# Optimization experiments

Measured on AMD Instinct MI355X. Metric: run time of the kernel, lower is better.

The kernel has to match this reference:

```python
import jax, jax.numpy as jnp
import numpy as np

B, C_IN, C_OUT, H, W = 16, 64, 64, 256, 256
M1, M2 = 32, 32  # retained Fourier modes (low-frequency corner block)


def setup_inputs() -> dict:
    key = jax.random.key(0)
    kx, kw, kb = jax.random.split(key, 3)
    x = jax.random.normal(kx, (B, C_IN, H, W), dtype=jnp.float32)
    # xavier_uniform over (in, out, m1, m2): fan_in = C_IN*M1*M2, fan_out = C_OUT*M1*M2
    bound = float(np.sqrt(6.0 / ((C_IN + C_OUT) * M1 * M2)))
    weights = jax.random.uniform(kw, (C_IN, C_OUT, M1, M2), jnp.float32, -bound, bound)
    bias = jax.random.normal(kb, (C_OUT,), dtype=jnp.float32) * 0.01
    return {"x": x, "weights": weights, "bias": bias}


def reference(x, weights, bias):
    # x: [B, Cin, H, W] real -> rFFT2 -> [B, Cin, H, W//2+1] complex
    x_ft = jnp.fft.rfft2(x, axes=(-2, -1))
    m1 = min(M1, x_ft.shape[-2])
    m2 = min(M2, x_ft.shape[-1])
    # Single fused complex-times-real channel mixing over the truncated mode block
    mixed = jnp.einsum("bixy,ioxy->boxy",
                       x_ft[:, :, :m1, :m2],
                       weights[:, :, :m1, :m2].astype(x_ft.dtype))
    out_ft = jnp.zeros((x.shape[0], weights.shape[1], x_ft.shape[-2], x_ft.shape[-1]),
                       dtype=x_ft.dtype)
    out_ft = out_ft.at[:, :, :m1, :m2].set(mixed)
    x_out = jnp.fft.irfft2(out_ft, s=(x.shape[-2], x.shape[-1]), axes=(-2, -1))
    return x_out + bias[None, :, None, None]
```

## Files before the change

kernel.cpp:

```cpp
#include <hip/hip_runtime.h>


#define H_ 256
#define W_ 256

typedef short short8 __attribute__((ext_vector_type(8)));
typedef float floatx4 __attribute__((ext_vector_type(4)));

static __device__ __forceinline__ unsigned short f2b(float f) {
    union { float f; unsigned int u; } v; v.f = f;
    unsigned int r = v.u + 0x7FFFu + ((v.u >> 16) & 1u);
    return (unsigned short)(r >> 16);
}

static __device__ __forceinline__ unsigned int cvt_pk_bf16(float a, float b) {
    unsigned int r;
    asm("v_cvt_pk_bf16_f32 %0, %1, %2" : "=v"(r) : "v"(a), "v"(b));
    return r;
}

__global__ void build_tables(unsigned short* ws) {
    int k = blockIdx.x;
    int n = threadIdx.x;
    int u = (k * n) & 255;
    double ang = 6.283185307179586476925286766559 * (double)u / 256.0;
    float c = (float)cos(ang), s = (float)sin(ang);
    unsigned short bc = f2b(c), bs = f2b(s), bns = f2b(-s);
    unsigned short* F2t = ws;
    unsigned short* F1e = ws + 16384;
    unsigned short* G1  = ws + 16384 + 32768;
    unsigned short* G2t = ws + 16384 + 65536;

    F2t[(2 * k) * 256 + n]     = bc;
    F2t[(2 * k + 1) * 256 + n] = bns;
    F1e[(2 * k) * 512 + 2 * n]         = bc;
    F1e[(2 * k) * 512 + 2 * n + 1]     = bs;
    F1e[(2 * k + 1) * 512 + 2 * n]     = bns;
    F1e[(2 * k + 1) * 512 + 2 * n + 1] = bc;
    G1[(2 * n) * 64 + 2 * k]         = bc;
    G1[(2 * n) * 64 + 2 * k + 1]     = bns;
    G1[(2 * n + 1) * 64 + 2 * k]     = bs;
    G1[(2 * n + 1) * 64 + 2 * k + 1] = bc;
    float fac = (k == 0) ? 1.f : 2.f;
    G2t[n * 64 + 2 * k]     = f2b(fac * c);
    G2t[n * 64 + 2 * k + 1] = f2b(-fac * s);
}

__global__ __launch_bounds__(256) void wtrans(const float* __restrict__ Wg,
                                              float* __restrict__ Wt) {
    __shared__ float t[64][65];
    const int iot = blockIdx.x;
    const int mt = blockIdx.y;
    const int tid = threadIdx.x;
    for (int q = 0; q < 16; ++q) {
        int idx = q * 256 + tid;
        int io = idx >> 6, m = idx & 63;
        t[io][m] = Wg[(size_t)(iot * 64 + io) * 1024 + mt * 64 + m];
    }
    __syncthreads();
    for (int q = 0; q < 16; ++q) {
        int idx = q * 256 + tid;
        int m = idx >> 6, io = idx & 63;
        Wt[(size_t)(mt * 64 + m) * 4096 + iot * 64 + io] = t[io][m];
    }
}

__global__ __launch_bounds__(256, 2) void fwd_kernel(const float* __restrict__ x,
                                                     const unsigned short* __restrict__ ws_u,
                                                     float* __restrict__ Y) {
    __shared__ __align__(16) unsigned short lA[64 * 264];
    __shared__ __align__(16) unsigned short lT[32 * 520];
    const int tid = threadIdx.x;
    const int wave = tid >> 6, lane = tid & 63;
    const int lm = lane & 15, lq = lane >> 4;
    const int bi = blockIdx.x;

    const float* xg = x + (size_t)bi * (H_ * W_);
    const unsigned short* F2tg = ws_u;
    const unsigned short* F1eg = ws_u + 16384;

    short8 bfA[8][4];
#pragma unroll
    for (int kk = 0; kk < 8; ++kk)
#pragma unroll
        for (int b = 0; b < 4; ++b)
            bfA[kk][b] = *(const short8*)(F2tg + (b * 16 + lm) * 256 + kk * 32 + lq * 8);

    floatx4 acc[4];
    for (int hc = 0; hc < 4; ++hc) {
        if (hc) __syncthreads();
#pragma unroll
        for (int j = 0; j < 16; ++j) {
            int fi = j * 256 + tid;
            int row = fi >> 6, c4 = fi & 63;
            const float4 v = *(const float4*)(xg + (hc * 64 + row) * 256 + c4 * 4);
            uint2 p;
            p.x = cvt_pk_bf16(v.x, v.y);
            p.y = cvt_pk_bf16(v.z, v.w);
            *(uint2*)(lA + row * 264 + c4 * 4) = p;
        }
        __syncthreads();
#pragma unroll
        for (int b = 0; b < 4; ++b) acc[b] = (floatx4){0.f, 0.f, 0.f, 0.f};
#pragma unroll
        for (int kk = 0; kk < 8; ++kk) {
            short8 af = *(const short8*)(lA + (wave * 16 + lm) * 264 + kk * 32 + lq * 8);
#pragma unroll
            for (int b = 0; b < 4; ++b)
                acc[b] = __builtin_amdgcn_mfma_f32_16x16x32_bf16(af, bfA[kk][b], acc[b], 0, 0, 0);
        }
#pragma unroll
        for (int b = 0; b < 4; ++b) {
            int col = b * 16 + lm;
            int ky = col >> 1, c = col & 1;
#pragma unroll
            for (int r = 0; r < 4; ++r) {
                int h = hc * 64 + wave * 16 + lq * 4 + r;
                lT[ky * 520 + 2 * h + c] = f2b(acc[b][r]);
            }
        }
    }
    __syncthreads();
    floatx4 acc2[2];
    acc2[0] = (floatx4){0.f, 0.f, 0.f, 0.f};
    acc2[1] = (floatx4){0.f, 0.f, 0.f, 0.f};
    for (int ks = 0; ks < 16; ++ks) {
        short8 af = *(const short8*)(F1eg + (wave * 16 + lm) * 512 + ks * 32 + lq * 8);
#pragma unroll
        for (int b = 0; b < 2; ++b) {
            short8 bf = *(const short8*)(lT + (b * 16 + lm) * 520 + ks * 32 + lq * 8);
            acc2[b] = __builtin_amdgcn_mfma_f32_16x16x32_bf16(af, bf, acc2[b], 0, 0, 0);
        }
    }
    float* Yg = Y + (size_t)bi * (64 * 32);
#pragma unroll
    for (int b = 0; b < 2; ++b) {
        int colk = b * 16 + lm;
        int mrow = wave * 16 + lq * 4;
#pragma unroll
        for (int r = 0; r < 4; ++r)
            Yg[(mrow + r) * 32 + colk] = acc2[b][r];
    }
}

__global__ __launch_bounds__(256) void mix_kernel(const float* __restrict__ Wt,
                                                  const float* __restrict__ Y,
                                                  unsigned short* __restrict__ Mx) {
    __shared__ float lW[64 * 64];
    __shared__ float lY[16 * 130];
    const int tid = threadIdx.x;
    const int bid = blockIdx.x;
    const int mode = (bid & 7) * 128 + (bid >> 3);
    const int kx = mode >> 5, ky = mode & 31;

    {
        const float4* src = (const float4*)(Wt + (size_t)mode * 4096);
        float4* dst = (float4*)lW;
        for (int q = 0; q < 4; ++q) dst[q * 256 + tid] = src[q * 256 + tid];
    }
    for (int q = 0; q < 8; ++q) {
        int e = q * 256 + tid;
        int b = e >> 7, r = e & 127;
        lY[b * 130 + r] = Y[(((size_t)b * 64 + (r >> 1)) * 64 + 2 * kx + (r & 1)) * 32 + ky];
    }
    __syncthreads();

    const int og = tid & 7;
    const int bc = tid >> 3;
    const int b = bc >> 1, c = bc & 1;
    float acc[8];
#pragma unroll
    for (int j = 0; j < 8; ++j) acc[j] = 0.f;
    for (int i = 0; i < 64; ++i) {
        float yv = lY[b * 130 + 2 * i + c];
        const floatx4 w0 = *(const floatx4*)&lW[i * 64 + og * 8];
        const floatx4 w1 = *(const floatx4*)&lW[i * 64 + og * 8 + 4];
        acc[0] += yv * w0[0]; acc[1] += yv * w0[1];
        acc[2] += yv * w0[2]; acc[3] += yv * w0[3];
        acc[4] += yv * w1[0]; acc[5] += yv * w1[1];
        acc[6] += yv * w1[2]; acc[7] += yv * w1[3];
    }
    const float scale = 1.f / 65536.f;
#pragma unroll
    for (int j = 0; j < 8; ++j) {
        int o = og * 8 + j;
        Mx[((size_t)(b * 64 + o) * 64 + 2 * kx + c) * 32 + ky] = f2b(acc[j] * scale);
    }
}

__global__ __launch_bounds__(256, 2) void inv_kernel(const unsigned short* __restrict__ ws_u,
                                                     const unsigned short* __restrict__ Mx,
                                                     const float* __restrict__ bias,
                                                     float* __restrict__ out) {
    __shared__ __align__(16) unsigned short lMx[32 * 64];
    __shared__ __align__(16) unsigned short lZ[256 * 72];
    __shared__ __align__(16) float lOut[32 * 260];
    const int tid = threadIdx.x;
    const int wave = tid >> 6, lane = tid & 63;
    const int lm = lane & 15, lq = lane >> 4;
    const int bo = blockIdx.x;
    const int o = bo & 63;

    const unsigned short* G1g = ws_u + 49152;
    const unsigned short* G2g = ws_u + 81920;
    const float bv = bias[o];

    short8 bfD[2][4];
#pragma unroll
    for (int ks = 0; ks < 2; ++ks)
#pragma unroll
        for (int b = 0; b < 4; ++b)
            bfD[ks][b] = *(const short8*)(G2g + ((wave * 4 + b) * 16 + lm) * 64 + ks * 32 + lq * 8);

    {
        short8 v = *(const short8*)(Mx + (size_t)bo * 2048 + tid * 8);
        int kx2 = tid >> 2, kyb = (tid & 3) * 8;
#pragma unroll
        for (int e = 0; e < 8; ++e)
            lMx[(kyb + e) * 64 + kx2] = (unsigned short)v[e];
    }
    __syncthreads();

    {
        floatx4 accc[8][2];
#pragma unroll
        for (int a = 0; a < 8; ++a)
#pragma unroll
            for (int b = 0; b < 2; ++b) accc[a][b] = (floatx4){0.f, 0.f, 0.f, 0.f};
#pragma unroll
        for (int ks = 0; ks < 2; ++ks) {
            short8 bf[2];
#pragma unroll
            for (int b = 0; b < 2; ++b)
                bf[b] = *(const short8*)(lMx + (b * 16 + lm) * 64 + ks * 32 + lq * 8);
#pragma unroll
            for (int a = 0; a < 8; ++a) {
                int mt = wave * 8 + a;
                short8 af = *(const short8*)(G1g + (mt * 16 + lm) * 64 + ks * 32 + lq * 8);
#pragma unroll
                for (int b = 0; b < 2; ++b)
                    accc[a][b] = __builtin_amdgcn_mfma_f32_16x16x32_bf16(af, bf[b], accc[a][b], 0, 0, 0);
            }
        }
#pragma unroll
        for (int a = 0; a < 8; ++a) {
            int mbase = (wave * 8 + a) * 16 + lq * 4;
#pragma unroll
            for (int b = 0; b < 2; ++b) {
                int ky = b * 16 + lm;
#pragma unroll
                for (int r = 0; r < 4; ++r) {
                    int m = mbase + r;
                    int h = m >> 1, c = m & 1;
                    lZ[h * 72 + 2 * ky + c] = f2b(accc[a][b][r]);
                }
            }
        }
    }
    __syncthreads();

    float* og = out + (size_t)bo * (H_ * W_);
    for (int s = 0; s < 4; ++s) {
        floatx4 accd[4][4];
#pragma unroll
        for (int a = 0; a < 4; ++a)
#pragma unroll
            for (int b = 0; b < 4; ++b) accd[a][b] = (floatx4){0.f, 0.f, 0.f, 0.f};
#pragma unroll
        for (int ks = 0; ks < 2; ++ks) {
            short8 af[4];
#pragma unroll
            for (int a = 0; a < 4; ++a) {
                int mt = s * 4 + a;
                af[a] = *(const short8*)(lZ + (mt * 16 + lm) * 72 + ks * 32 + lq * 8);
            }
#pragma unroll
            for (int a = 0; a < 4; ++a)
#pragma unroll
                for (int b = 0; b < 4; ++b)
                    accd[a][b] = __builtin_amdgcn_mfma_f32_16x16x32_bf16(af[a], bfD[ks][b], accd[a][b], 0, 0, 0);
        }
        for (int g = 0; g < 2; ++g) {
            __syncthreads();
#pragma unroll
            for (int a2 = 0; a2 < 2; ++a2) {
                int a = g * 2 + a2;
#pragma unroll
                for (int b = 0; b < 4; ++b) {
                    int col = wave * 64 + b * 16 + lm;
#pragma unroll
                    for (int r = 0; r < 4; ++r) {
                        int row = a2 * 16 + lq * 4 + r;
                        lOut[row * 260 + col] = accd[a][b][r] + bv;
                    }
                }
            }
            __syncthreads();
#pragma unroll
            for (int j = 0; j < 8; ++j) {
                int row = wave * 8 + j;
                floatx4 v = *(const floatx4*)(lOut + row * 260 + lane * 4);
                *(floatx4*)(og + (s * 64 + g * 32 + row) * 256 + lane * 4) = v;
            }
        }
    }
}

extern "C" void kernel_launch(void* const* d_in, const int* in_sizes, int n_in,
                              void* d_out, int out_size, void* d_ws, size_t ws_size,
                              hipStream_t stream) {
    const float* x    = (const float*)d_in[0];
    const float* w    = (const float*)d_in[1];
    const float* bias = (const float*)d_in[2];
    float* out = (float*)d_out;
    unsigned short* ws_u = (unsigned short*)d_ws;
    float* Y  = (float*)((char*)d_ws + 196608);
    unsigned short* Mx = (unsigned short*)((char*)d_ws + 8585216);
    float* Wt = (float*)((char*)d_ws + 33554432);

    build_tables<<<32, 256, 0, stream>>>(ws_u);
    wtrans<<<dim3(64, 16), 256, 0, stream>>>(w, Wt);
    fwd_kernel<<<1024, 256, 0, stream>>>(x, ws_u, Y);
    mix_kernel<<<1024, 256, 0, stream>>>(Wt, Y, Mx);
    inv_kernel<<<1024, 256, 0, stream>>>(ws_u, Mx, bias, out);
}
```

Measured before the change: 505.3 us.

## Prefetch next x chunk into registers, stream DFT table, store inverse output directly

The forward kernel now prefetches the next 64-row chunk of x into registers while converting the current chunk, overlapping global loads with the MFMA work. It no longer holds the whole F2 table in registers and instead reloads those fragments from global or cache inside the MFMA loop, trading register pressure for extra loads. The inverse kernel drops its LDS staging buffer and the two barriers around it, writing accumulator values plus bias straight to global memory. Those direct writes are scattered scalar stores (16 consecutive floats per lane group) rather than the coalesced float4 rows they replace, which may lower write efficiency.

```diff
diff --git a/kernel.cpp b/kernel.cpp
--- a/kernel.cpp
+++ b/kernel.cpp
@@ -79,12 +79,13 @@
     const unsigned short* F2tg = ws_u;
     const unsigned short* F1eg = ws_u + 16384;
 
-    short8 bfA[8][4];
-#pragma unroll
-    for (int kk = 0; kk < 8; ++kk)
-#pragma unroll
-        for (int b = 0; b < 4; ++b)
-            bfA[kk][b] = *(const short8*)(F2tg + (b * 16 + lm) * 256 + kk * 32 + lq * 8);
+    float4 pv[16];
+#pragma unroll
+    for (int j = 0; j < 16; ++j) {
+        int fi = j * 256 + tid;
+        int row = fi >> 6, c4 = fi & 63;
+        pv[j] = *(const float4*)(xg + row * 256 + c4 * 4);
+    }
 
     floatx4 acc[4];
     for (int hc = 0; hc < 4; ++hc) {
@@ -93,11 +94,12 @@
         for (int j = 0; j < 16; ++j) {
             int fi = j * 256 + tid;
             int row = fi >> 6, c4 = fi & 63;
-            const float4 v = *(const float4*)(xg + (hc * 64 + row) * 256 + c4 * 4);
             uint2 p;
-            p.x = cvt_pk_bf16(v.x, v.y);
-            p.y = cvt_pk_bf16(v.z, v.w);
+            p.x = cvt_pk_bf16(pv[j].x, pv[j].y);
+            p.y = cvt_pk_bf16(pv[j].z, pv[j].w);
             *(uint2*)(lA + row * 264 + c4 * 4) = p;
+            if (hc < 3)
+                pv[j] = *(const float4*)(xg + ((hc + 1) * 64 + row) * 256 + c4 * 4);
         }
         __syncthreads();
 #pragma unroll
@@ -106,8 +108,10 @@
         for (int kk = 0; kk < 8; ++kk) {
             short8 af = *(const short8*)(lA + (wave * 16 + lm) * 264 + kk * 32 + lq * 8);
 #pragma unroll
-            for (int b = 0; b < 4; ++b)
-                acc[b] = __builtin_amdgcn_mfma_f32_16x16x32_bf16(af, bfA[kk][b], acc[b], 0, 0, 0);
+            for (int b = 0; b < 4; ++b) {
+                short8 bf = *(const short8*)(F2tg + (b * 16 + lm) * 256 + kk * 32 + lq * 8);
+                acc[b] = __builtin_amdgcn_mfma_f32_16x16x32_bf16(af, bf, acc[b], 0, 0, 0);
+            }
         }
 #pragma unroll
         for (int b = 0; b < 4; ++b) {
@@ -194,7 +198,6 @@
                                                      float* __restrict__ out) {
     __shared__ __align__(16) unsigned short lMx[32 * 64];
     __shared__ __align__(16) unsigned short lZ[256 * 72];
-    __shared__ __align__(16) float lOut[32 * 260];
     const int tid = threadIdx.x;
     const int wave = tid >> 6, lane = tid & 63;
     const int lm = lane & 15, lq = lane >> 4;
@@ -280,27 +283,15 @@
                 for (int b = 0; b < 4; ++b)
                     accd[a][b] = __builtin_amdgcn_mfma_f32_16x16x32_bf16(af[a], bfD[ks][b], accd[a][b], 0, 0, 0);
         }
-        for (int g = 0; g < 2; ++g) {
-            __syncthreads();
-#pragma unroll
-            for (int a2 = 0; a2 < 2; ++a2) {
-                int a = g * 2 + a2;
-#pragma unroll
-                for (int b = 0; b < 4; ++b) {
-                    int col = wave * 64 + b * 16 + lm;
-#pragma unroll
-                    for (int r = 0; r < 4; ++r) {
-                        int row = a2 * 16 + lq * 4 + r;
-                        lOut[row * 260 + col] = accd[a][b][r] + bv;
-                    }
-                }
-            }
-            __syncthreads();
-#pragma unroll
-            for (int j = 0; j < 8; ++j) {
-                int row = wave * 8 + j;
-                floatx4 v = *(const floatx4*)(lOut + row * 260 + lane * 4);
-                *(floatx4*)(og + (s * 64 + g * 32 + row) * 256 + lane * 4) = v;
+#pragma unroll
+        for (int a = 0; a < 4; ++a) {
+            int hbase = (s * 4 + a) * 16 + lq * 4;
+#pragma unroll
+            for (int b = 0; b < 4; ++b) {
+                int w = (wave * 4 + b) * 16 + lm;
+#pragma unroll
+                for (int r = 0; r < 4; ++r)
+                    og[(hbase + r) * 256 + w] = accd[a][b][r] + bv;
             }
         }
     }
```

Result: slower. 534.8 us (+5.8%).
